# Kernel tuning notes

Measured on AMD Instinct MI355X. Metric: run time of the kernel, lower is better.

The kernel has to match this reference:

```python
import jax, jax.numpy as jnp
import numpy as np

NUM_CODES = 1024
CODE_DIM = 64
N_TOKENS = 131072
DECAY = 0.99
EPS = 1e-5


def setup_inputs() -> dict:
    key = jax.random.key(0)
    k1, k2, k3, k4 = jax.random.split(key, 4)
    return {
        "z": jax.random.normal(k1, (N_TOKENS, CODE_DIM), dtype=jnp.float32),
        "codebook": jax.random.normal(k2, (NUM_CODES, CODE_DIM), dtype=jnp.float32),
        "cluster_size": jax.random.uniform(k3, (NUM_CODES,), dtype=jnp.float32),
        "ema_w": jax.random.normal(k4, (NUM_CODES, CODE_DIM), dtype=jnp.float32),
    }


def reference(z, codebook, cluster_size, ema_w):
    # Squared L2 distances; argmin over squared distances == argmin over cdist.
    # d2: [N, K]
    d2 = (
        jnp.sum(z * z, axis=-1, keepdims=True)
        - 2.0 * (z @ codebook.T)
        + jnp.sum(codebook * codebook, axis=-1)
    )
    indices = jnp.argmin(d2, axis=-1)          # [N] int
    quantized = codebook[indices]              # [N, D]

    # EMA statistics (torch version uses one_hot; segment_sum is the fused
    # equivalent without materializing the [N, K] one-hot matrix).
    counts = jax.ops.segment_sum(jnp.ones_like(indices, dtype=z.dtype), indices,
                                 num_segments=NUM_CODES)          # encodings.sum(0)
    dw = jax.ops.segment_sum(z, indices, num_segments=NUM_CODES)  # encodings.T @ z

    new_cluster_size = DECAY * cluster_size + (1.0 - DECAY) * counts
    new_ema_w = DECAY * ema_w + (1.0 - DECAY) * dw
    n = jnp.sum(new_cluster_size)
    cs = (new_cluster_size + EPS) / (n + NUM_CODES * EPS) * n
    new_codebook = new_ema_w / cs[:, None]

    commitment_loss = jnp.mean((z - jax.lax.stop_gradient(quantized)) ** 2)
    quantized_st = z + jax.lax.stop_gradient(quantized - z)  # straight-through

    return quantized_st, indices, commitment_loss, new_codebook, new_cluster_size, new_ema_w
```

## Files before the change

kernel.cpp:

```cpp
#include <hip/hip_runtime.h>
#include <hip/hip_bf16.h>


#define DECAY 0.99f
#define OMD   0.01f
#define EPSV  1e-5f
#define BIASF 192.0f

typedef __attribute__((ext_vector_type(8))) __bf16 bf16x8;
typedef __attribute__((ext_vector_type(4))) float  float4v;

static __device__ __forceinline__ unsigned short bfbits(float f) {
    __bf16 h = (__bf16)f;
    return __builtin_bit_cast(unsigned short, h);
}
static __device__ __forceinline__ bf16x8 cvt8(float4v a, float4v b) {
    bf16x8 r;
    r[0] = (__bf16)a[0]; r[1] = (__bf16)a[1]; r[2] = (__bf16)a[2]; r[3] = (__bf16)a[3];
    r[4] = (__bf16)b[0]; r[5] = (__bf16)b[1]; r[6] = (__bf16)b[2]; r[7] = (__bf16)b[3];
    return r;
}

static __device__ __forceinline__ int dec_idx(unsigned key, int quad) {
    int iter = key & 255;
    return ((iter >> 6) << 8) + (((iter >> 2) & 15) << 4) + (quad << 2) + (iter & 3);
}

__global__ void vq_prep(const float* __restrict__ cb,
                        float* __restrict__ wsf, int* __restrict__ wsi,
                        int K, int NT) {
    int t = blockIdx.x * 256 + threadIdx.x;
    if (t < K) {
        wsi[t] = 0;
        const float4v* cp = (const float4v*)(cb + (size_t)t * 64);
        float s = 0.f;
        #pragma unroll
        for (int i = 0; i < 16; ++i) {
            float4v v = cp[i];
            s += v[0] * v[0] + v[1] * v[1] + v[2] * v[2] + v[3] * v[3];
        }
        wsf[K + t] = BIASF - 0.5f * s;
    }
    if (t == 0) wsf[2 * K] = 0.f;
}

__launch_bounds__(512)
__global__ void vq_assign(const float* __restrict__ z,
                          const float* __restrict__ cb,
                          float* __restrict__ wsf, int* __restrict__ wsi,
                          float* __restrict__ out,
                          int NT, int K) {
    __shared__ __align__(16) unsigned short cbs[256 * 72];
    __shared__ float cns[256];
    __shared__ int hist[1024];

    const int tid  = threadIdx.x;
    const int lane = tid & 63;
    const int wave = tid >> 6;
    const int col  = lane & 15;
    const int quad = lane >> 4;
    const int wtok0 = blockIdx.x * 256 + wave * 32;
    const float* cnormp = wsf + K;
    const bool smallK = (K <= 1024);

    for (int i = tid; i < 1024; i += 512) hist[i] = 0;

    bf16x8 bf0[2], bf1[2];
    #pragma unroll
    for (int g = 0; g < 2; ++g) {
        int tok = wtok0 + g * 16 + col;
        if (tok >= NT) tok = NT - 1;
        const float* zp = z + (size_t)tok * 64 + quad * 8;
        float4v f0 = *(const float4v*)(zp);
        float4v f1 = *(const float4v*)(zp + 4);
        float4v f2 = *(const float4v*)(zp + 32);
        float4v f3 = *(const float4v*)(zp + 36);
        bf0[g] = cvt8(f0, f1);
        bf1[g] = cvt8(f2, f3);
    }

    unsigned k1[2] = { 0u, 0u }, k2[2] = { 0u, 0u };
    const unsigned kmask = 0xFFFFFF00u;
    const int nchunk = (K + 255) >> 8;

    for (int c = 0; c < nchunk; ++c) {
        #pragma unroll
        for (int i = 0; i < 8; ++i) {
            int f4 = (i * 512 + tid) * 4;
            int row = f4 >> 6, d = f4 & 63;
            int code = c * 256 + row;
            uint2 p;
            if (code < K) {
                float4v v = *(const float4v*)(cb + (size_t)code * 64 + d);
                p.x = (unsigned int)bfbits(v[0]) | ((unsigned int)bfbits(v[1]) << 16);
                p.y = (unsigned int)bfbits(v[2]) | ((unsigned int)bfbits(v[3]) << 16);
            } else { p.x = 0u; p.y = 0u; }
            *(uint2*)(&cbs[row * 72 + d]) = p;
        }
        if (tid < 256) {
            int code = c * 256 + tid;
            cns[tid] = (code < K) ? cnormp[code] : 0.0f;
        }
        __syncthreads();

        #pragma unroll 4
        for (int t = 0; t < 16; ++t) {
            const unsigned short* arow = cbs + (t * 16 + col) * 72;
            bf16x8 a0 = *(const bf16x8*)(arow + quad * 8);
            bf16x8 a1 = *(const bf16x8*)(arow + 32 + quad * 8);
            float4v cni = *(const float4v*)(cns + t * 16 + quad * 4);
            const int iterbase = (c << 6) | (t << 2);
            #pragma unroll
            for (int g = 0; g < 2; ++g) {
                float4v acc = cni;
                acc = __builtin_amdgcn_mfma_f32_16x16x32_bf16(a0, bf0[g], acc, 0, 0, 0);
                acc = __builtin_amdgcn_mfma_f32_16x16x32_bf16(a1, bf1[g], acc, 0, 0, 0);
                #pragma unroll
                for (int r = 0; r < 4; ++r) {
                    unsigned kb = (__float_as_uint(acc[r]) & kmask) | (unsigned)(iterbase + r);
                    unsigned lo = k2[g] > kb ? k2[g] : kb;
                    k2[g] = k1[g] < lo ? k1[g] : lo;
                    k1[g] = k1[g] > kb ? k1[g] : kb;
                }
            }
        }
        __syncthreads();
    }

    int ibst[2];
    #pragma unroll
    for (int g = 0; g < 2; ++g) {
        int tok = wtok0 + g * 16 + col;
        if (tok >= NT) tok = NT - 1;
        int ia = dec_idx(k1[g], quad);
        int ib = dec_idx(k2[g], quad);
        int cand[8];
        #pragma unroll
        for (int q = 0; q < 4; ++q) {
            cand[2 * q]     = __shfl(ia, q * 16 + col, 64);
            cand[2 * q + 1] = __shfl(ib, q * 16 + col, 64);
        }
        const float* zr = z + (size_t)tok * 64 + quad * 16;
        float4v zv0 = *(const float4v*)(zr);
        float4v zv1 = *(const float4v*)(zr + 4);
        float4v zv2 = *(const float4v*)(zr + 8);
        float4v zv3 = *(const float4v*)(zr + 12);
        double ps[8];
        #pragma unroll
        for (int s = 0; s < 8; ++s) {
            int cc = (cand[s] < K) ? cand[s] : 0;
            const float* cr = cb + (size_t)cc * 64 + quad * 16;
            float4v c0 = *(const float4v*)(cr);
            float4v c1 = *(const float4v*)(cr + 4);
            float4v c2 = *(const float4v*)(cr + 8);
            float4v c3 = *(const float4v*)(cr + 12);
            double a = 0.0;
            #pragma unroll
            for (int j = 0; j < 4; ++j) {
                double e0 = (double)zv0[j] - (double)c0[j];
                double e1 = (double)zv1[j] - (double)c1[j];
                double e2 = (double)zv2[j] - (double)c2[j];
                double e3 = (double)zv3[j] - (double)c3[j];
                a = fma(e0, e0, a); a = fma(e1, e1, a);
                a = fma(e2, e2, a); a = fma(e3, e3, a);
            }
            ps[s] = (cand[s] < K) ? a : 1.0e300;
        }
        #pragma unroll
        for (int s = 0; s < 8; ++s) {
            ps[s] += __shfl_xor(ps[s], 16, 64);
            ps[s] += __shfl_xor(ps[s], 32, 64);
        }
        double bs = ps[0]; int bi = cand[0];
        #pragma unroll
        for (int s = 1; s < 8; ++s) {
            if (ps[s] < bs || (ps[s] == bs && cand[s] < bi)) { bs = ps[s]; bi = cand[s]; }
        }
        ibst[g] = bi;
    }

    const size_t off_idx = (size_t)NT * 64;

    if (lane < 32) {
        int tk = wtok0 + lane;
        if (tk < NT) {
            int ib = (lane < 16) ? ibst[0] : ibst[1];
            out[off_idx + tk] = (float)ib;
            if (smallK) atomicAdd(&hist[ib], 1);
            else        atomicAdd(&wsi[ib], 1);
        }
    }

    __syncthreads();
    if (smallK) {
        for (int k = tid; k < K; k += 512) {
            int c = hist[k];
            if (c) atomicAdd(&wsi[k], c);
        }
    }
}

__launch_bounds__(1024)
__global__ void vq_quant(const float* __restrict__ z,
                         const float* __restrict__ cb,
                         const float* __restrict__ out_idx,
                         float* __restrict__ out,
                         float* __restrict__ lossp, int NT) {
    __shared__ float red[16];
    const int tid  = threadIdx.x;
    const int lane = tid & 63;
    const int wave = tid >> 6;
    const int gt   = blockIdx.x * 1024 + tid;

    float lsum = 0.f;
    if (gt < NT * 16) {
        int token = gt >> 4, seg = gt & 15;
        int idx = (int)out_idx[token];
        const float4v zf = *(const float4v*)(z  + (size_t)token * 64 + seg * 4);
        const float4v qf = *(const float4v*)(cb + (size_t)idx   * 64 + seg * 4);
        *(float4v*)(out + (size_t)token * 64 + seg * 4) = qf;
        float e0 = zf[0] - qf[0], e1 = zf[1] - qf[1];
        float e2 = zf[2] - qf[2], e3 = zf[3] - qf[3];
        lsum = e0 * e0 + e1 * e1 + e2 * e2 + e3 * e3;
    }
    #pragma unroll
    for (int off = 1; off < 64; off <<= 1) lsum += __shfl_xor(lsum, off, 64);
    if (lane == 0) red[wave] = lsum;
    __syncthreads();
    if (tid == 0) {
        float s = 0.f;
        #pragma unroll
        for (int i = 0; i < 16; ++i) s += red[i];
        atomicAdd(lossp, s);
    }
}

__launch_bounds__(512)
__global__ void vq_dwred(const float* __restrict__ z,
                         const float* __restrict__ out_idx,
                         const float* __restrict__ cs,
                         float* __restrict__ wsf, const int* __restrict__ wsi,
                         float* __restrict__ partial,
                         float* __restrict__ out,
                         int NT, int K, int nchunks) {
    extern __shared__ float acc[];
    __shared__ float red[8];

    const int tid   = threadIdx.x;
    const int lane  = tid & 63;
    const int wave  = tid >> 6;
    const int chunk = blockIdx.x >> 2;
    const int g     = blockIdx.x & 3;
    const int tsub  = lane >> 4;
    const int d     = lane & 15;
    const size_t KD = (size_t)K * 64;

    for (int i = tid; i < K * 16; i += 512) acc[i] = 0.f;

    if (blockIdx.x == 0) {
        float part = 0.f;
        for (int k = tid; k < K; k += 512)
            part += DECAY * cs[k] + OMD * (float)wsi[k];
        #pragma unroll
        for (int off = 1; off < 64; off <<= 1) part += __shfl_xor(part, off, 64);
        if (lane == 0) red[wave] = part;
        __syncthreads();
        if (tid == 0) {
            float nn = 0.f;
            #pragma unroll
            for (int i = 0; i < 8; ++i) nn += red[i];
            wsf[2 * K + 1] = nn;
            out[(size_t)NT * 64 + NT] = wsf[2 * K] / ((float)NT * 64.0f);
        }
    }
    __syncthreads();

    const int C  = (NT + nchunks - 1) / nchunks;
    const int T0 = chunk * C;
    const int T1 = (T0 + C < NT) ? (T0 + C) : NT;
    const float* zs = z + g * 16 + d;

    #pragma unroll 4
    for (int t = T0 + wave * 4 + tsub; t < T1; t += 32) {
        float v   = zs[(size_t)t * 64];
        int  code = (int)out_idx[t];
        atomicAdd(&acc[code * 16 + d], v);
    }
    __syncthreads();

    float* pb = partial + (size_t)chunk * KD + g * 16;
    for (int i = tid; i < K * 16; i += 512) {
        int k = i >> 4, dd = i & 15;
        pb[(size_t)k * 64 + dd] = acc[i];
    }
}

__global__ void vq_final(const float* __restrict__ cs,
                         const float* __restrict__ ema,
                         const float* __restrict__ wsf,
                         const int* __restrict__ wsi,
                         const float* __restrict__ partial,
                         float* __restrict__ out, int NT, int K, int S) {
    const int KD = K * 64;
    int t = blockIdx.x * 256 + threadIdx.x;
    if (t >= KD) return;
    const int k = t >> 6;
    const float n = wsf[2 * K + 1];
    float d0 = 0.f, d1 = 0.f, d2 = 0.f, d3 = 0.f;
    float d4 = 0.f, d5 = 0.f, d6 = 0.f, d7 = 0.f;
    int s = 0;
    for (; s + 8 <= S; s += 8) {
        d0 += partial[(size_t)(s + 0) * KD + t];
        d1 += partial[(size_t)(s + 1) * KD + t];
        d2 += partial[(size_t)(s + 2) * KD + t];
        d3 += partial[(size_t)(s + 3) * KD + t];
        d4 += partial[(size_t)(s + 4) * KD + t];
        d5 += partial[(size_t)(s + 5) * KD + t];
        d6 += partial[(size_t)(s + 6) * KD + t];
        d7 += partial[(size_t)(s + 7) * KD + t];
    }
    for (; s < S; ++s) d0 += partial[(size_t)s * KD + t];
    const float dsum = ((d0 + d1) + (d2 + d3)) + ((d4 + d5) + (d6 + d7));
    const float dw = DECAY * ema[t] + OMD * dsum;
    const float ncs = DECAY * cs[k] + OMD * (float)wsi[k];
    const float csn = (ncs + EPSV) / (n + (float)K * EPSV) * n;
    const size_t off_cb  = (size_t)NT * 64 + NT + 1;
    const size_t off_cs  = off_cb + (size_t)KD;
    const size_t off_ema = off_cs + K;
    out[off_cb  + t] = dw / csn;
    out[off_ema + t] = dw;
    if ((t & 63) == 0) out[off_cs + k] = ncs;
}

extern "C" void kernel_launch(void* const* d_in, const int* in_sizes, int n_in,
                              void* d_out, int out_size, void* d_ws, size_t ws_size,
                              hipStream_t stream) {
    const float* z   = (const float*)d_in[0];
    const float* cb  = (const float*)d_in[1];
    const float* cs  = (const float*)d_in[2];
    const float* ema = (const float*)d_in[3];
    float* out = (float*)d_out;
    float* wsf = (float*)d_ws;
    int*   wsi = (int*)d_ws;

    const int NT = in_sizes[0] / 64;
    const int K  = in_sizes[2];
    const int KD = K * 64;

    size_t avail = ws_size / 4;
    int nchunks = 128;
    while (nchunks > 1 && (size_t)2 * K + 2 + (size_t)nchunks * KD > avail)
        nchunks >>= 1;

    float* partial = wsf + 2 * K + 2;
    const size_t dwlds = (size_t)K * 16 * sizeof(float);

    vq_prep<<<(K + 255) / 256, 256, 0, stream>>>(cb, wsf, wsi, K, NT);
    vq_assign<<<(NT + 255) / 256, 512, 0, stream>>>(z, cb, wsf, wsi, out, NT, K);
    vq_quant<<<(NT * 16 + 1023) / 1024, 1024, 0, stream>>>(
        z, cb, out + (size_t)NT * 64, out, wsf + 2 * K, NT);
    vq_dwred<<<nchunks * 4, 512, dwlds, stream>>>(
        z, out + (size_t)NT * 64, cs, wsf, wsi, partial, out, NT, K, nchunks);
    vq_final<<<(KD + 255) / 256, 256, 0, stream>>>(cs, ema, wsf, wsi, partial,
                                                   out, NT, K, nchunks);
}
```

Baseline: 242.2 us.

## Fuse quantized gather and loss into segment reduction, shrink codebook LDS chunk

Removes the separate vq_quant kernel. Its work (gathering the quantized codebook rows, writing them out, and reducing the commitment loss) moves into vq_dwred, which already reads z and the indices, so z is read once fewer from global memory and one launch goes away. The loss mean is now written by vq_final. Separately, vq_assign stages the codebook in chunks of 128 codes instead of 256, with adjusted index encoding and decoding, to cut LDS use. The number of dw reduction chunks is halved. The fused loop now does scalar codebook loads and output stores per element, which may make that kernel heavier.

```diff
diff --git a/kernel.cpp b/kernel.cpp
--- a/kernel.cpp
+++ b/kernel.cpp
@@ -6,6 +6,7 @@
 #define OMD   0.01f
 #define EPSV  1e-5f
 #define BIASF 192.0f
+#define KCH   128
 
 typedef __attribute__((ext_vector_type(8))) __bf16 bf16x8;
 typedef __attribute__((ext_vector_type(4))) float  float4v;
@@ -23,7 +24,7 @@
 
 static __device__ __forceinline__ int dec_idx(unsigned key, int quad) {
     int iter = key & 255;
-    return ((iter >> 6) << 8) + (((iter >> 2) & 15) << 4) + (quad << 2) + (iter & 3);
+    return ((iter >> 2) << 4) + (quad << 2) + (iter & 3);
 }
 
 __global__ void vq_prep(const float* __restrict__ cb,
@@ -50,8 +51,8 @@
                           float* __restrict__ wsf, int* __restrict__ wsi,
                           float* __restrict__ out,
                           int NT, int K) {
-    __shared__ __align__(16) unsigned short cbs[256 * 72];
-    __shared__ float cns[256];
+    __shared__ __align__(16) unsigned short cbs[KCH * 72];
+    __shared__ float cns[KCH];
     __shared__ int hist[1024];
 
     const int tid  = threadIdx.x;
@@ -81,14 +82,14 @@
 
     unsigned k1[2] = { 0u, 0u }, k2[2] = { 0u, 0u };
     const unsigned kmask = 0xFFFFFF00u;
-    const int nchunk = (K + 255) >> 8;
+    const int nchunk = (K + KCH - 1) / KCH;
 
     for (int c = 0; c < nchunk; ++c) {
         #pragma unroll
-        for (int i = 0; i < 8; ++i) {
+        for (int i = 0; i < 4; ++i) {
             int f4 = (i * 512 + tid) * 4;
             int row = f4 >> 6, d = f4 & 63;
-            int code = c * 256 + row;
+            int code = c * KCH + row;
             uint2 p;
             if (code < K) {
                 float4v v = *(const float4v*)(cb + (size_t)code * 64 + d);
@@ -97,19 +98,19 @@
             } else { p.x = 0u; p.y = 0u; }
             *(uint2*)(&cbs[row * 72 + d]) = p;
         }
-        if (tid < 256) {
-            int code = c * 256 + tid;
+        if (tid < KCH) {
+            int code = c * KCH + tid;
             cns[tid] = (code < K) ? cnormp[code] : 0.0f;
         }
         __syncthreads();
 
         #pragma unroll 4
-        for (int t = 0; t < 16; ++t) {
+        for (int t = 0; t < KCH / 16; ++t) {
             const unsigned short* arow = cbs + (t * 16 + col) * 72;
             bf16x8 a0 = *(const bf16x8*)(arow + quad * 8);
             bf16x8 a1 = *(const bf16x8*)(arow + 32 + quad * 8);
             float4v cni = *(const float4v*)(cns + t * 16 + quad * 4);
-            const int iterbase = (c << 6) | (t << 2);
+            const int iterbase = ((c * (KCH / 16) + t) << 2);
             #pragma unroll
             for (int g = 0; g < 2; ++g) {
                 float4v acc = cni;
@@ -200,43 +201,9 @@
     }
 }
 
-__launch_bounds__(1024)
-__global__ void vq_quant(const float* __restrict__ z,
-                         const float* __restrict__ cb,
-                         const float* __restrict__ out_idx,
-                         float* __restrict__ out,
-                         float* __restrict__ lossp, int NT) {
-    __shared__ float red[16];
-    const int tid  = threadIdx.x;
-    const int lane = tid & 63;
-    const int wave = tid >> 6;
-    const int gt   = blockIdx.x * 1024 + tid;
-
-    float lsum = 0.f;
-    if (gt < NT * 16) {
-        int token = gt >> 4, seg = gt & 15;
-        int idx = (int)out_idx[token];
-        const float4v zf = *(const float4v*)(z  + (size_t)token * 64 + seg * 4);
-        const float4v qf = *(const float4v*)(cb + (size_t)idx   * 64 + seg * 4);
-        *(float4v*)(out + (size_t)token * 64 + seg * 4) = qf;
-        float e0 = zf[0] - qf[0], e1 = zf[1] - qf[1];
-        float e2 = zf[2] - qf[2], e3 = zf[3] - qf[3];
-        lsum = e0 * e0 + e1 * e1 + e2 * e2 + e3 * e3;
-    }
-    #pragma unroll
-    for (int off = 1; off < 64; off <<= 1) lsum += __shfl_xor(lsum, off, 64);
-    if (lane == 0) red[wave] = lsum;
-    __syncthreads();
-    if (tid == 0) {
-        float s = 0.f;
-        #pragma unroll
-        for (int i = 0; i < 16; ++i) s += red[i];
-        atomicAdd(lossp, s);
-    }
-}
-
 __launch_bounds__(512)
 __global__ void vq_dwred(const float* __restrict__ z,
+                         const float* __restrict__ cb,
                          const float* __restrict__ out_idx,
                          const float* __restrict__ cs,
                          float* __restrict__ wsf, const int* __restrict__ wsi,
@@ -270,7 +237,6 @@
             #pragma unroll
             for (int i = 0; i < 8; ++i) nn += red[i];
             wsf[2 * K + 1] = nn;
-            out[(size_t)NT * 64 + NT] = wsf[2 * K] / ((float)NT * 64.0f);
         }
     }
     __syncthreads();
@@ -278,15 +244,31 @@
     const int C  = (NT + nchunks - 1) / nchunks;
     const int T0 = chunk * C;
     const int T1 = (T0 + C < NT) ? (T0 + C) : NT;
-    const float* zs = z + g * 16 + d;
-
+    const int doff = g * 16 + d;
+    const float* zs = z + doff;
+
+    float lsum = 0.f;
     #pragma unroll 4
     for (int t = T0 + wave * 4 + tsub; t < T1; t += 32) {
         float v   = zs[(size_t)t * 64];
         int  code = (int)out_idx[t];
+        float q   = cb[(size_t)code * 64 + doff];
+        out[(size_t)t * 64 + doff] = q;
+        float e = v - q;
+        lsum += e * e;
         atomicAdd(&acc[code * 16 + d], v);
     }
+    #pragma unroll
+    for (int off = 1; off < 64; off <<= 1) lsum += __shfl_xor(lsum, off, 64);
     __syncthreads();
+    if (lane == 0) red[wave] = lsum;
+    __syncthreads();
+    if (tid == 0) {
+        float s = 0.f;
+        #pragma unroll
+        for (int i = 0; i < 8; ++i) s += red[i];
+        atomicAdd(&wsf[2 * K], s);
+    }
 
     float* pb = partial + (size_t)chunk * KD + g * 16;
     for (int i = tid; i < K * 16; i += 512) {
@@ -303,6 +285,7 @@
                          float* __restrict__ out, int NT, int K, int S) {
     const int KD = K * 64;
     int t = blockIdx.x * 256 + threadIdx.x;
+    if (t == 0) out[(size_t)NT * 64 + NT] = wsf[2 * K] / ((float)NT * 64.0f);
     if (t >= KD) return;
     const int k = t >> 6;
     const float n = wsf[2 * K + 1];
@@ -348,7 +331,7 @@
     const int KD = K * 64;
 
     size_t avail = ws_size / 4;
-    int nchunks = 128;
+    int nchunks = 64;
     while (nchunks > 1 && (size_t)2 * K + 2 + (size_t)nchunks * KD > avail)
         nchunks >>= 1;
 
@@ -357,10 +340,8 @@
 
     vq_prep<<<(K + 255) / 256, 256, 0, stream>>>(cb, wsf, wsi, K, NT);
     vq_assign<<<(NT + 255) / 256, 512, 0, stream>>>(z, cb, wsf, wsi, out, NT, K);
-    vq_quant<<<(NT * 16 + 1023) / 1024, 1024, 0, stream>>>(
-        z, cb, out + (size_t)NT * 64, out, wsf + 2 * K, NT);
     vq_dwred<<<nchunks * 4, 512, dwlds, stream>>>(
-        z, out + (size_t)NT * 64, cs, wsf, wsi, partial, out, NT, K, nchunks);
+        z, cb, out + (size_t)NT * 64, cs, wsf, wsi, partial, out, NT, K, nchunks);
     vq_final<<<(KD + 255) / 256, 256, 0, stream>>>(cs, ema, wsf, wsi, partial,
                                                    out, NT, K, nchunks);
 }
```

Result: faster. 209.0 us (-13.7%).
